# Kernel tuning notes

Measured on AMD Instinct MI355X. Metric: run time of the kernel, lower is better.

The kernel has to match this reference:

```python
import jax, jax.numpy as jnp
import numpy as np

# Ordered bi-bi mechanism, species order per _build_species_list:
# [E, EA, EQ, EAB, A, B, P, Q] -> indices 0..7
# Transitions: E+A<->EA, EA+B<->EAB, EAB<->EQ+P, EQ<->E+Q (all reversible)
N_SPECIES = 8
N_TRANS = 4

# forward: rate * [enzyme] * prod([substrates]); -1 = no factor (padded)
ENZ_F = np.array([0, 1, 3, 2], dtype=np.int32)          # E, EA, EAB, EQ
SUB_F = np.array([[4], [5], [-1], [-1]], dtype=np.int32)  # A, B, -, -
# reverse: rate * [to-enzyme] * prod([products])
ENZ_R = np.array([1, 3, 2, 0], dtype=np.int32)          # EA, EAB, EQ, E
PROD_R = np.array([[-1], [-1], [6], [7]], dtype=np.int32)  # -, -, P, Q
REV_MASK = np.array([1.0, 1.0, 1.0, 1.0], dtype=np.float32)

# Stoichiometry (n_trans, n_species), applied as dydt += v_net[:,None]*S[i]
S_FORWARD = np.array([
    [-1,  1,  0,  0, -1,  0,  0,  0],
    [ 0, -1,  0,  1,  0, -1,  0,  0],
    [ 0,  0,  1, -1,  0,  0,  1,  0],
    [ 1,  0, -1,  0,  0,  0,  0,  1],
], dtype=np.float32)


def _masked_gather_prod(y, idx):
    # y: (B, n_species); idx: (n_trans, k) with -1 padding
    safe = jnp.maximum(idx, 0)
    g = y[:, safe.reshape(-1)].reshape(y.shape[0], idx.shape[0], idx.shape[1])  # (B,T,k)
    g = jnp.where(idx[None, :, :] >= 0, g, 1.0)
    return jnp.prod(g, axis=-1)  # (B, T)


def setup_inputs() -> dict:
    key = jax.random.key(0)
    k1, k2, k3 = jax.random.split(key, 3)
    B = 2_000_000
    return {
        "t": jnp.zeros((1,), dtype=jnp.float32),
        "y": jax.random.uniform(k1, (B, N_SPECIES), dtype=jnp.float32),
        "forward_rates": jax.random.uniform(k2, (B, N_TRANS), dtype=jnp.float32),
        "reverse_rates": jax.random.uniform(k3, (B, N_TRANS), dtype=jnp.float32),
    }


def reference(t, y, forward_rates, reverse_rates):
    enz_f = jnp.asarray(ENZ_F)
    enz_r = jnp.asarray(ENZ_R)
    sub_f = jnp.asarray(SUB_F)
    prod_r = jnp.asarray(PROD_R)
    S = jnp.asarray(S_FORWARD)
    rev_mask = jnp.asarray(REV_MASK)

    # v_forward[b,i] = k_f[b,i] * y[b, enz_f[i]] * prod_j y[b, sub_f[i,j]]
    v_f = forward_rates * y[:, enz_f] * _masked_gather_prod(y, sub_f)
    # v_reverse analogous, zeroed for irreversible transitions
    v_r = reverse_rates * y[:, enz_r] * _masked_gather_prod(y, prod_r) * rev_mask[None, :]
    v_net = v_f - v_r  # (B, T)
    # dydt[b,s] = sum_i v_net[b,i] * S[i,s]
    return jnp.einsum("bt,ts->bs", v_net, S)
```

## Files before the change

kernel.cpp:

```cpp
#include <hip/hip_runtime.h>


typedef float v4f __attribute__((ext_vector_type(4)));

#define ITERS 4

__device__ __forceinline__ void ode_elem(v4f ya, v4f yb, v4f f, v4f r,
                                         v4f& oa, v4f& ob) {
    float E  = ya.x, EA = ya.y, EQ = ya.z, EAB = ya.w;
    float A  = yb.x, Bc = yb.y, P  = yb.z, Q   = yb.w;

    float v0 = f.x * E   * A  - r.x * EA;
    float v1 = f.y * EA  * Bc - r.y * EAB;
    float v2 = f.z * EAB      - r.z * EQ * P;
    float v3 = f.w * EQ       - r.w * E  * Q;

    oa.x = v3 - v0;
    oa.y = v0 - v1;
    oa.z = v2 - v3;
    oa.w = v1 - v2;
    ob.x = -v0;
    ob.y = -v1;
    ob.z =  v2;
    ob.w =  v3;
}

__global__ __launch_bounds__(256) void ode_kernel(
    const v4f* __restrict__ y4,
    const v4f* __restrict__ kf4,
    const v4f* __restrict__ kr4,
    v4f* __restrict__ out4,
    int B)
{
    const int stride = gridDim.x * blockDim.x;
    const int e0 = blockIdx.x * blockDim.x + threadIdx.x;

    if (e0 + (ITERS - 1) * stride < B) {
        v4f ya[ITERS], yb[ITERS], f[ITERS], r[ITERS];
        #pragma unroll
        for (int k = 0; k < ITERS; ++k) {
            int e = e0 + k * stride;
            ya[k] = __builtin_nontemporal_load(y4 + 2 * e);
            yb[k] = __builtin_nontemporal_load(y4 + 2 * e + 1);
            f[k]  = __builtin_nontemporal_load(kf4 + e);
            r[k]  = __builtin_nontemporal_load(kr4 + e);
        }

        v4f oa[ITERS], ob[ITERS];
        #pragma unroll
        for (int k = 0; k < ITERS; ++k)
            ode_elem(ya[k], yb[k], f[k], r[k], oa[k], ob[k]);

        #pragma unroll
        for (int k = 0; k < ITERS; ++k) {
            int e = e0 + k * stride;
            out4[2 * e]     = oa[k];
            out4[2 * e + 1] = ob[k];
        }
    } else {
        for (int k = 0; k < ITERS; ++k) {
            int e = e0 + k * stride;
            if (e < B) {
                v4f ya = __builtin_nontemporal_load(y4 + 2 * e);
                v4f yb = __builtin_nontemporal_load(y4 + 2 * e + 1);
                v4f f  = __builtin_nontemporal_load(kf4 + e);
                v4f r  = __builtin_nontemporal_load(kr4 + e);
                v4f oa, ob;
                ode_elem(ya, yb, f, r, oa, ob);
                out4[2 * e]     = oa;
                out4[2 * e + 1] = ob;
            }
        }
    }
}

extern "C" void kernel_launch(void* const* d_in, const int* in_sizes, int n_in,
                              void* d_out, int out_size, void* d_ws, size_t ws_size,
                              hipStream_t stream) {
    const v4f* y4  = (const v4f*)d_in[1];
    const v4f* kf4 = (const v4f*)d_in[2];
    const v4f* kr4 = (const v4f*)d_in[3];
    v4f* out4 = (v4f*)d_out;
    int B = in_sizes[1] / 8;

    int block = 256;
    int grid  = (B + block * ITERS - 1) / (block * ITERS);
    ode_kernel<<<grid, block, 0, stream>>>(y4, kf4, kr4, out4, B);
}
```

Before: 165.2 us.

## Switch to persistent grid-stride loop with software-pipelined prefetch

Replaces the fixed 4-element-per-thread batch with a persistent grid of 2048 blocks that loops over elements and prefetches the next element's inputs before computing and storing the current one. It also drops the nontemporal load hints and adds an occupancy hint to launch bounds. The aim is to overlap load latency with compute and stores while cutting block launch overhead. In exchange each thread has only one load in flight ahead instead of four, which may lower memory-level parallelism on a bandwidth-bound kernel.

```diff
diff --git a/kernel.cpp b/kernel.cpp
--- a/kernel.cpp
+++ b/kernel.cpp
@@ -2,8 +2,6 @@
 
 
 typedef float v4f __attribute__((ext_vector_type(4)));
-
-#define ITERS 4
 
 __device__ __forceinline__ void ode_elem(v4f ya, v4f yb, v4f f, v4f r,
                                          v4f& oa, v4f& ob) {
@@ -25,52 +23,43 @@
     ob.w =  v3;
 }
 
-__global__ __launch_bounds__(256) void ode_kernel(
+__global__ __launch_bounds__(256, 8) void ode_kernel(
     const v4f* __restrict__ y4,
     const v4f* __restrict__ kf4,
     const v4f* __restrict__ kr4,
     v4f* __restrict__ out4,
     int B)
 {
-    const int stride = gridDim.x * blockDim.x;
-    const int e0 = blockIdx.x * blockDim.x + threadIdx.x;
+    const int T = gridDim.x * blockDim.x;
+    int e = blockIdx.x * blockDim.x + threadIdx.x;
 
-    if (e0 + (ITERS - 1) * stride < B) {
-        v4f ya[ITERS], yb[ITERS], f[ITERS], r[ITERS];
-        #pragma unroll
-        for (int k = 0; k < ITERS; ++k) {
-            int e = e0 + k * stride;
-            ya[k] = __builtin_nontemporal_load(y4 + 2 * e);
-            yb[k] = __builtin_nontemporal_load(y4 + 2 * e + 1);
-            f[k]  = __builtin_nontemporal_load(kf4 + e);
-            r[k]  = __builtin_nontemporal_load(kr4 + e);
+    bool v = e < B;
+    v4f ya, yb, f, r;
+    if (v) {
+        ya = y4[2 * e];
+        yb = y4[2 * e + 1];
+        f  = kf4[e];
+        r  = kr4[e];
+    }
+
+    while (v) {
+        int  en = e + T;
+        bool vn = en < B;
+        v4f yan, ybn, fn, rn;
+        if (vn) {
+            yan = y4[2 * en];
+            ybn = y4[2 * en + 1];
+            fn  = kf4[en];
+            rn  = kr4[en];
         }
 
-        v4f oa[ITERS], ob[ITERS];
-        #pragma unroll
-        for (int k = 0; k < ITERS; ++k)
-            ode_elem(ya[k], yb[k], f[k], r[k], oa[k], ob[k]);
+        v4f oa, ob;
+        ode_elem(ya, yb, f, r, oa, ob);
+        out4[2 * e]     = oa;
+        out4[2 * e + 1] = ob;
 
-        #pragma unroll
-        for (int k = 0; k < ITERS; ++k) {
-            int e = e0 + k * stride;
-            out4[2 * e]     = oa[k];
-            out4[2 * e + 1] = ob[k];
-        }
-    } else {
-        for (int k = 0; k < ITERS; ++k) {
-            int e = e0 + k * stride;
-            if (e < B) {
-                v4f ya = __builtin_nontemporal_load(y4 + 2 * e);
-                v4f yb = __builtin_nontemporal_load(y4 + 2 * e + 1);
-                v4f f  = __builtin_nontemporal_load(kf4 + e);
-                v4f r  = __builtin_nontemporal_load(kr4 + e);
-                v4f oa, ob;
-                ode_elem(ya, yb, f, r, oa, ob);
-                out4[2 * e]     = oa;
-                out4[2 * e + 1] = ob;
-            }
-        }
+        e = en; v = vn;
+        ya = yan; yb = ybn; f = fn; r = rn;
     }
 }
 
@@ -84,6 +73,8 @@
     int B = in_sizes[1] / 8;
 
     int block = 256;
-    int grid  = (B + block * ITERS - 1) / (block * ITERS);
+    int grid  = 2048;
+    int maxg  = (B + block - 1) / block;
+    if (grid > maxg) grid = maxg;
     ode_kernel<<<grid, block, 0, stream>>>(y4, kf4, kr4, out4, B);
 }
```

Measured after the change: 171.9 us. +4.1%, slower.
